# Kernel tuning notes

Measured on AMD Instinct MI355X. Metric: run time of the kernel, lower is better.

The kernel has to match this reference:

```python
import jax, jax.numpy as jnp
import numpy as np

HOP_NUM = 3
N_NODES = 40000
N_EDGES = 640000
IN_DIM = 128
N_ALPHAS = HOP_NUM * (HOP_NUM + 1) // 2  # triangular layerRegular params


def setup_inputs() -> dict:
    key = jax.random.key(0)
    k_h, k_d, k_a, k_s, k_t = jax.random.split(key, 5)
    h = jax.random.normal(k_h, (N_NODES, IN_DIM), dtype=jnp.float32)
    d = jax.random.uniform(k_d, (N_NODES,), dtype=jnp.float32)  # degree normalization per node
    alphas = jax.random.uniform(k_a, (N_ALPHAS,), dtype=jnp.float32)
    src = jax.random.randint(k_s, (N_EDGES,), 0, N_NODES, dtype=jnp.int32)
    dst = jax.random.randint(k_t, (N_EDGES,), 0, N_NODES, dtype=jnp.int32)
    return {"h": h, "d": d, "alphas": alphas, "src": src, "dst": dst}


def reference(h, d, alphas, src, dst):
    n = h.shape[0]
    # edge_applying: e = 1 * d[dst] * d[src]  (symmetric-normalized edge weight)
    e = d[dst] * d[src]                      # [E]
    outs = [h]
    k = 0
    for i in range(HOP_NUM):
        feat = h
        for q in range(i + 1):
            # update_all(u_mul_e('h','e'), sum): agg[v] = sum_{(u,v)} feat[u] * e
            msg = feat[src] * e[:, None]     # [E, D]
            agg = jax.ops.segment_sum(msg, dst, num_segments=n)  # [N, D]
            a = alphas[k]; k += 1
            feat = agg * a + (1.0 - a) * feat
            # feature_drop with p=0.0 (eval) is identity
        outs.append(feat)
    return jnp.concatenate(outs, axis=1)       # [N, (HOP_NUM+1)*D]
```

## Files before the change

kernel.cpp:

```cpp
#include <hip/hip_runtime.h>


#define NN  40000
#define NE  640000
#define CAP 64

__device__ inline unsigned short f2h(float f) {
    _Float16 h = (_Float16)f;
    return *(unsigned short*)&h;
}
__device__ inline float h2f(unsigned short u) {
    _Float16 h = *(_Float16*)&u;
    return (float)h;
}
__device__ inline unsigned short f2bf(float f) {
    unsigned int x = __float_as_uint(f);
    x += 0x7fffu + ((x >> 16) & 1u);
    return (unsigned short)(x >> 16);
}
__device__ inline unsigned int pack_bf2(float x, float y) {
    return ((unsigned int)f2bf(y) << 16) | (unsigned int)f2bf(x);
}
__device__ inline float bflo(unsigned int u) { return __uint_as_float(u << 16); }
__device__ inline float bfhi(unsigned int u) { return __uint_as_float(u & 0xffff0000u); }

__global__ __launch_bounds__(256) void build_buckets_k(
    const int* __restrict__ src, const int* __restrict__ dst,
    const float* __restrict__ deg,
    int* __restrict__ counts, unsigned int* __restrict__ buck) {
    int e = blockIdx.x * 256 + threadIdx.x;
    if (e >= NE) return;
    int s = src[e];
    int v = dst[e];
    int slot = atomicAdd(&counts[v], 1);
    if (slot < CAP) {
        float w = deg[s] * deg[v];
        buck[v * CAP + slot] = ((unsigned int)f2h(w) << 16) | (unsigned int)s;
    }
}

__global__ __launch_bounds__(256) void cvt_h_k(
    const float* __restrict__ h, unsigned int* __restrict__ hb) {
    int i = blockIdx.x * 256 + threadIdx.x;
    if (i >= NN * 64) return;
    float2 f = *(const float2*)(h + (size_t)i * 2);
    hb[i] = pack_bf2(f.x, f.y);
}

__device__ inline float2 gather_node(
    const unsigned int* __restrict__ feat,
    const int* __restrict__ counts, const unsigned int* __restrict__ buck,
    int v, int lane) {
    int cnt = counts[v];
    if (cnt > CAP) cnt = CAP;
    unsigned int myw = buck[(size_t)v * CAP + lane];
    if (lane >= cnt) myw = 0u;
    float ax = 0.f, ay = 0.f, bx = 0.f, by = 0.f;
    for (int j = 0; j < cnt; j += 4) {
        unsigned int u0 = __shfl(myw, j + 0);
        unsigned int u1 = __shfl(myw, j + 1);
        unsigned int u2 = __shfl(myw, j + 2);
        unsigned int u3 = __shfl(myw, j + 3);
        unsigned int f0 = feat[(size_t)(u0 & 0xffffu) * 64 + lane];
        unsigned int f1 = feat[(size_t)(u1 & 0xffffu) * 64 + lane];
        unsigned int f2 = feat[(size_t)(u2 & 0xffffu) * 64 + lane];
        unsigned int f3 = feat[(size_t)(u3 & 0xffffu) * 64 + lane];
        float w0 = h2f((unsigned short)(u0 >> 16));
        float w1 = h2f((unsigned short)(u1 >> 16));
        float w2 = h2f((unsigned short)(u2 >> 16));
        float w3 = h2f((unsigned short)(u3 >> 16));
        ax = fmaf(w0, bflo(f0), ax); ay = fmaf(w0, bfhi(f0), ay);
        bx = fmaf(w1, bflo(f1), bx); by = fmaf(w1, bfhi(f1), by);
        ax = fmaf(w2, bflo(f2), ax); ay = fmaf(w2, bfhi(f2), ay);
        bx = fmaf(w3, bflo(f3), bx); by = fmaf(w3, bfhi(f3), by);
    }
    return make_float2(ax + bx, ay + by);
}

__global__ __launch_bounds__(256) void agg_k(
    const unsigned int* __restrict__ feat,
    const int* __restrict__ counts, const unsigned int* __restrict__ buck,
    unsigned int* __restrict__ outf) {
    int gid  = blockIdx.x * 256 + threadIdx.x;
    int v    = gid >> 6;
    int lane = gid & 63;
    if (v >= NN) return;
    float2 acc = gather_node(feat, counts, buck, v, lane);
    outf[(size_t)v * 64 + lane] = pack_bf2(acc.x, acc.y);
}

__global__ __launch_bounds__(256) void agg3_fused_k(
    const unsigned int* __restrict__ p2b,
    const float* __restrict__ h,
    const unsigned int* __restrict__ p1b,
    const int* __restrict__ counts, const unsigned int* __restrict__ buck,
    const float* __restrict__ alphas, float* __restrict__ out) {
    int gid  = blockIdx.x * 256 + threadIdx.x;
    int v    = gid >> 6;
    int lane = gid & 63;
    if (v >= NN) return;
    float2 p3 = gather_node(p2b, counts, buck, v, lane);

    float a0 = alphas[0], a1 = alphas[1], a2 = alphas[2];
    float a3 = alphas[3], a4 = alphas[4], a5 = alphas[5];
    float c1p = a0, c1h = 1.f - a0;
    float c2pp = a2 * a1;
    float c2p  = a2 * (1.f - a1) + (1.f - a2) * a1;
    float c2h  = (1.f - a2) * (1.f - a1);
    float s2pp = a4 * a3;
    float s2p  = a4 * (1.f - a3) + (1.f - a4) * a3;
    float s2h  = (1.f - a4) * (1.f - a3);
    float c3ppp = a5 * s2pp;
    float c3pp  = a5 * s2p + (1.f - a5) * s2pp;
    float c3p   = a5 * s2h + (1.f - a5) * s2p;
    float c3h   = (1.f - a5) * s2h;

    int i2 = lane * 2;
    float2 hf = *(const float2*)(h + (size_t)v * 128 + i2);
    unsigned int u1 = p1b[(size_t)v * 64 + lane];
    unsigned int u2 = p2b[(size_t)v * 64 + lane];
    float q1x = bflo(u1), q1y = bfhi(u1);
    float q2x = bflo(u2), q2y = bfhi(u2);

    float2 r1, r2, r3;
    r1.x = c1p * q1x + c1h * hf.x;
    r1.y = c1p * q1y + c1h * hf.y;
    r2.x = c2pp * q2x + c2p * q1x + c2h * hf.x;
    r2.y = c2pp * q2y + c2p * q1y + c2h * hf.y;
    r3.x = c3ppp * p3.x + c3pp * q2x + c3p * q1x + c3h * hf.x;
    r3.y = c3ppp * p3.y + c3pp * q2y + c3p * q1y + c3h * hf.y;

    float* o = out + (size_t)v * 512;
    *(float2*)(o + i2)       = hf;
    *(float2*)(o + 128 + i2) = r1;
    *(float2*)(o + 256 + i2) = r2;
    *(float2*)(o + 384 + i2) = r3;
}

extern "C" void kernel_launch(void* const* d_in, const int* in_sizes, int n_in,
                              void* d_out, int out_size, void* d_ws, size_t ws_size,
                              hipStream_t stream) {
    const float* h      = (const float*)d_in[0];
    const float* deg    = (const float*)d_in[1];
    const float* alphas = (const float*)d_in[2];
    const int*   src    = (const int*)d_in[3];
    const int*   dst    = (const int*)d_in[4];
    float* out = (float*)d_out;

    char* ws = (char*)d_ws;
    int*          counts = (int*)(ws + 0);
    unsigned int* buck   = (unsigned int*)(ws + 160000);
    unsigned int* hb     = (unsigned int*)(ws + 10400000);
    unsigned int* p1b    = (unsigned int*)(ws + 20640000);
    unsigned int* p2b    = (unsigned int*)(ws + 30880000);

    hipMemsetAsync(counts, 0, NN * sizeof(int), stream);
    build_buckets_k<<<NE / 256, 256, 0, stream>>>(src, dst, deg, counts, buck);
    cvt_h_k<<<(NN * 64 + 255) / 256, 256, 0, stream>>>(h, hb);

    agg_k<<<NN / 4, 256, 0, stream>>>(hb,  counts, buck, p1b);
    agg_k<<<NN / 4, 256, 0, stream>>>(p1b, counts, buck, p2b);
    agg3_fused_k<<<NN / 4, 256, 0, stream>>>(p2b, h, p1b, counts, buck,
                                             alphas, out);
}
```

Measured before the change: 216.1 us.

## Merge bucket build with bf16 conversion and use scalar bucket loads in gather

Fuses the edge-bucketing kernel and the bf16 conversion of h into a single launch by partitioning the grid by block index, which removes one kernel launch. In the gather, the node index is made wave-uniform with readfirstlane, so bucket entries are read as uniform (scalar) loads instead of a per-lane load followed by shuffles. The loop is unrolled to 8 neighbours with four accumulator pairs to keep more feature loads in flight. Out-of-range slots are masked to node 0 with zero weight, which adds some wasted loads when a bucket count is not a multiple of 8.

Result: no change. 212.4 us (-1.7%).

```diff
diff --git a/kernel.cpp b/kernel.cpp
--- a/kernel.cpp
+++ b/kernel.cpp
@@ -24,57 +24,69 @@
 __device__ inline float bflo(unsigned int u) { return __uint_as_float(u << 16); }
 __device__ inline float bfhi(unsigned int u) { return __uint_as_float(u & 0xffff0000u); }
 
-__global__ __launch_bounds__(256) void build_buckets_k(
+__global__ __launch_bounds__(256) void build_cvt_k(
     const int* __restrict__ src, const int* __restrict__ dst,
-    const float* __restrict__ deg,
-    int* __restrict__ counts, unsigned int* __restrict__ buck) {
-    int e = blockIdx.x * 256 + threadIdx.x;
-    if (e >= NE) return;
-    int s = src[e];
-    int v = dst[e];
-    int slot = atomicAdd(&counts[v], 1);
-    if (slot < CAP) {
-        float w = deg[s] * deg[v];
-        buck[v * CAP + slot] = ((unsigned int)f2h(w) << 16) | (unsigned int)s;
+    const float* __restrict__ deg, const float* __restrict__ h,
+    int* __restrict__ counts, unsigned int* __restrict__ buck,
+    unsigned int* __restrict__ hb) {
+    int b = blockIdx.x;
+    if (b < NE / 256) {
+        int e = b * 256 + threadIdx.x;
+        int s = src[e];
+        int v = dst[e];
+        int slot = atomicAdd(&counts[v], 1);
+        if (slot < CAP) {
+            float w = deg[s] * deg[v];
+            buck[v * CAP + slot] = ((unsigned int)f2h(w) << 16) | (unsigned int)s;
+        }
+    } else {
+        int i = (b - NE / 256) * 256 + threadIdx.x;
+        if (i < NN * 64) {
+            float2 f = *(const float2*)(h + (size_t)i * 2);
+            hb[i] = pack_bf2(f.x, f.y);
+        }
     }
-}
-
-__global__ __launch_bounds__(256) void cvt_h_k(
-    const float* __restrict__ h, unsigned int* __restrict__ hb) {
-    int i = blockIdx.x * 256 + threadIdx.x;
-    if (i >= NN * 64) return;
-    float2 f = *(const float2*)(h + (size_t)i * 2);
-    hb[i] = pack_bf2(f.x, f.y);
 }
 
 __device__ inline float2 gather_node(
     const unsigned int* __restrict__ feat,
     const int* __restrict__ counts, const unsigned int* __restrict__ buck,
     int v, int lane) {
-    int cnt = counts[v];
+    int vs = __builtin_amdgcn_readfirstlane(v);
+    int cnt = counts[vs];
     if (cnt > CAP) cnt = CAP;
-    unsigned int myw = buck[(size_t)v * CAP + lane];
-    if (lane >= cnt) myw = 0u;
+    const unsigned int* brow = buck + (size_t)vs * CAP;
+
     float ax = 0.f, ay = 0.f, bx = 0.f, by = 0.f;
-    for (int j = 0; j < cnt; j += 4) {
-        unsigned int u0 = __shfl(myw, j + 0);
-        unsigned int u1 = __shfl(myw, j + 1);
-        unsigned int u2 = __shfl(myw, j + 2);
-        unsigned int u3 = __shfl(myw, j + 3);
-        unsigned int f0 = feat[(size_t)(u0 & 0xffffu) * 64 + lane];
-        unsigned int f1 = feat[(size_t)(u1 & 0xffffu) * 64 + lane];
-        unsigned int f2 = feat[(size_t)(u2 & 0xffffu) * 64 + lane];
-        unsigned int f3 = feat[(size_t)(u3 & 0xffffu) * 64 + lane];
-        float w0 = h2f((unsigned short)(u0 >> 16));
-        float w1 = h2f((unsigned short)(u1 >> 16));
-        float w2 = h2f((unsigned short)(u2 >> 16));
-        float w3 = h2f((unsigned short)(u3 >> 16));
-        ax = fmaf(w0, bflo(f0), ax); ay = fmaf(w0, bfhi(f0), ay);
-        bx = fmaf(w1, bflo(f1), bx); by = fmaf(w1, bfhi(f1), by);
-        ax = fmaf(w2, bflo(f2), ax); ay = fmaf(w2, bfhi(f2), ay);
-        bx = fmaf(w3, bflo(f3), bx); by = fmaf(w3, bfhi(f3), by);
+    float cx = 0.f, cy = 0.f, dx = 0.f, dy = 0.f;
+    for (int j = 0; j < cnt; j += 8) {
+        unsigned int uu[8];
+#pragma unroll
+        for (int k = 0; k < 8; ++k) uu[k] = brow[j + k];
+        float wj[8]; int sj[8];
+#pragma unroll
+        for (int k = 0; k < 8; ++k) {
+            bool ok = (j + k) < cnt;
+            wj[k] = ok ? h2f((unsigned short)(uu[k] >> 16)) : 0.f;
+            sj[k] = ok ? (int)(uu[k] & 0xffffu) : 0;
+        }
+        unsigned int fj[8];
+#pragma unroll
+        for (int k = 0; k < 8; ++k)
+            fj[k] = feat[(size_t)sj[k] * 64 + lane];
+#pragma unroll
+        for (int k = 0; k < 8; k += 4) {
+            ax = fmaf(wj[k + 0], bflo(fj[k + 0]), ax);
+            ay = fmaf(wj[k + 0], bfhi(fj[k + 0]), ay);
+            bx = fmaf(wj[k + 1], bflo(fj[k + 1]), bx);
+            by = fmaf(wj[k + 1], bfhi(fj[k + 1]), by);
+            cx = fmaf(wj[k + 2], bflo(fj[k + 2]), cx);
+            cy = fmaf(wj[k + 2], bfhi(fj[k + 2]), cy);
+            dx = fmaf(wj[k + 3], bflo(fj[k + 3]), dx);
+            dy = fmaf(wj[k + 3], bfhi(fj[k + 3]), dy);
+        }
     }
-    return make_float2(ax + bx, ay + by);
+    return make_float2((ax + bx) + (cx + dx), (ay + by) + (cy + dy));
 }
 
 __global__ __launch_bounds__(256) void agg_k(
@@ -155,8 +167,8 @@
     unsigned int* p2b    = (unsigned int*)(ws + 30880000);
 
     hipMemsetAsync(counts, 0, NN * sizeof(int), stream);
-    build_buckets_k<<<NE / 256, 256, 0, stream>>>(src, dst, deg, counts, buck);
-    cvt_h_k<<<(NN * 64 + 255) / 256, 256, 0, stream>>>(h, hb);
+    build_cvt_k<<<NE / 256 + (NN * 64 + 255) / 256, 256, 0, stream>>>(
+        src, dst, deg, h, counts, buck, hb);
 
     agg_k<<<NN / 4, 256, 0, stream>>>(hb,  counts, buck, p1b);
     agg_k<<<NN / 4, 256, 0, stream>>>(p1b, counts, buck, p2b);
```

## Split bf16 feature tables into column chunks so gathers stay cache-resident

Applied to the files above, without the earlier changes.

Stores the bf16 node features as four 32-column chunk tables of 8-byte entries and assigns blocks so that the gather for each chunk touches a smaller working set (about 2.5 MB per chunk), aiming for better L2/MALL hit rates. Each node is now handled by 8 lanes per chunk instead of a full wave, with bucket entries read directly in pairs rather than broadcast by shuffles. Nontemporal loads and stores are used for streaming edge lists, buckets and output. The bucket list is re-read once per chunk, and the block-index mapping interleaves chunks, which may spread concurrent work across chunks and weaken the locality it aims for.

Result: slower. 295.4 us (+36.7%).

```diff
diff --git a/kernel.cpp b/kernel.cpp
--- a/kernel.cpp
+++ b/kernel.cpp
@@ -4,6 +4,12 @@
 #define NN  40000
 #define NE  640000
 #define CAP 64
+#define NCH 4
+#define CW  8
+
+typedef unsigned int uint;
+typedef unsigned long long u64;
+typedef float f32x4 __attribute__((ext_vector_type(4)));
 
 __device__ inline unsigned short f2h(float f) {
     _Float16 h = (_Float16)f;
@@ -14,92 +20,98 @@
     return (float)h;
 }
 __device__ inline unsigned short f2bf(float f) {
-    unsigned int x = __float_as_uint(f);
+    uint x = __float_as_uint(f);
     x += 0x7fffu + ((x >> 16) & 1u);
     return (unsigned short)(x >> 16);
 }
-__device__ inline unsigned int pack_bf2(float x, float y) {
-    return ((unsigned int)f2bf(y) << 16) | (unsigned int)f2bf(x);
+__device__ inline uint pack_bf2(float x, float y) {
+    return ((uint)f2bf(y) << 16) | (uint)f2bf(x);
 }
-__device__ inline float bflo(unsigned int u) { return __uint_as_float(u << 16); }
-__device__ inline float bfhi(unsigned int u) { return __uint_as_float(u & 0xffff0000u); }
+__device__ inline float bflo(uint u) { return __uint_as_float(u << 16); }
+__device__ inline float bfhi(uint u) { return __uint_as_float(u & 0xffff0000u); }
 
-__global__ __launch_bounds__(256) void build_buckets_k(
+__global__ __launch_bounds__(256) void build_k(
     const int* __restrict__ src, const int* __restrict__ dst,
     const float* __restrict__ deg,
-    int* __restrict__ counts, unsigned int* __restrict__ buck) {
+    int* __restrict__ counts, uint* __restrict__ buck) {
     int e = blockIdx.x * 256 + threadIdx.x;
-    if (e >= NE) return;
-    int s = src[e];
-    int v = dst[e];
+    int s = __builtin_nontemporal_load(src + e);
+    int v = __builtin_nontemporal_load(dst + e);
     int slot = atomicAdd(&counts[v], 1);
     if (slot < CAP) {
         float w = deg[s] * deg[v];
-        buck[v * CAP + slot] = ((unsigned int)f2h(w) << 16) | (unsigned int)s;
+        __builtin_nontemporal_store(((uint)f2h(w) << 16) | (uint)s,
+                                    &buck[v * CAP + slot]);
     }
 }
 
-__global__ __launch_bounds__(256) void cvt_h_k(
-    const float* __restrict__ h, unsigned int* __restrict__ hb) {
-    int i = blockIdx.x * 256 + threadIdx.x;
-    if (i >= NN * 64) return;
-    float2 f = *(const float2*)(h + (size_t)i * 2);
-    hb[i] = pack_bf2(f.x, f.y);
+__global__ __launch_bounds__(256) void cvt_k(
+    const float* __restrict__ h, u64* __restrict__ tab) {
+    int b  = blockIdx.x;
+    int c  = (b & 7) >> 1;
+    int wi = (b >> 3) * 2 + (b & 1);
+    int t  = wi * 256 + threadIdx.x;
+    int v  = t >> 3, w8 = t & 7;
+    f32x4 hv = __builtin_nontemporal_load(
+        (const f32x4*)(h + (size_t)v * 128 + c * 32 + w8 * 4));
+    u64 o = ((u64)pack_bf2(hv.z, hv.w) << 32) | (u64)pack_bf2(hv.x, hv.y);
+    tab[(size_t)c * NN * CW + t] = o;
 }
 
-__device__ inline float2 gather_node(
-    const unsigned int* __restrict__ feat,
-    const int* __restrict__ counts, const unsigned int* __restrict__ buck,
-    int v, int lane) {
+__device__ inline void gather_chunk(
+    const u64* __restrict__ tab, const int* __restrict__ counts,
+    const uint* __restrict__ buck, int v, int w8, float acc[4]) {
     int cnt = counts[v];
     if (cnt > CAP) cnt = CAP;
-    unsigned int myw = buck[(size_t)v * CAP + lane];
-    if (lane >= cnt) myw = 0u;
-    float ax = 0.f, ay = 0.f, bx = 0.f, by = 0.f;
-    for (int j = 0; j < cnt; j += 4) {
-        unsigned int u0 = __shfl(myw, j + 0);
-        unsigned int u1 = __shfl(myw, j + 1);
-        unsigned int u2 = __shfl(myw, j + 2);
-        unsigned int u3 = __shfl(myw, j + 3);
-        unsigned int f0 = feat[(size_t)(u0 & 0xffffu) * 64 + lane];
-        unsigned int f1 = feat[(size_t)(u1 & 0xffffu) * 64 + lane];
-        unsigned int f2 = feat[(size_t)(u2 & 0xffffu) * 64 + lane];
-        unsigned int f3 = feat[(size_t)(u3 & 0xffffu) * 64 + lane];
-        float w0 = h2f((unsigned short)(u0 >> 16));
-        float w1 = h2f((unsigned short)(u1 >> 16));
-        float w2 = h2f((unsigned short)(u2 >> 16));
-        float w3 = h2f((unsigned short)(u3 >> 16));
-        ax = fmaf(w0, bflo(f0), ax); ay = fmaf(w0, bfhi(f0), ay);
-        bx = fmaf(w1, bflo(f1), bx); by = fmaf(w1, bfhi(f1), by);
-        ax = fmaf(w2, bflo(f2), ax); ay = fmaf(w2, bfhi(f2), ay);
-        bx = fmaf(w3, bflo(f3), bx); by = fmaf(w3, bfhi(f3), by);
+    const u64* brow = (const u64*)(buck + (size_t)v * CAP);
+    acc[0] = acc[1] = acc[2] = acc[3] = 0.f;
+    for (int j = 0; j < cnt; j += 2) {
+        u64 b01 = __builtin_nontemporal_load(brow + (j >> 1));
+        uint b0 = (uint)b01, b1 = (uint)(b01 >> 32);
+        bool ok1 = (j + 1) < cnt;
+        float w0 = h2f((unsigned short)(b0 >> 16));
+        float w1 = ok1 ? h2f((unsigned short)(b1 >> 16)) : 0.f;
+        int s0 = (int)(b0 & 0xffffu);
+        int s1 = ok1 ? (int)(b1 & 0xffffu) : 0;
+        u64 f0 = tab[(size_t)s0 * CW + w8];
+        u64 f1 = tab[(size_t)s1 * CW + w8];
+        uint f0l = (uint)f0, f0h = (uint)(f0 >> 32);
+        uint f1l = (uint)f1, f1h = (uint)(f1 >> 32);
+        acc[0] = fmaf(w0, bflo(f0l), acc[0]); acc[1] = fmaf(w0, bfhi(f0l), acc[1]);
+        acc[2] = fmaf(w0, bflo(f0h), acc[2]); acc[3] = fmaf(w0, bfhi(f0h), acc[3]);
+        acc[0] = fmaf(w1, bflo(f1l), acc[0]); acc[1] = fmaf(w1, bfhi(f1l), acc[1]);
+        acc[2] = fmaf(w1, bflo(f1h), acc[2]); acc[3] = fmaf(w1, bfhi(f1h), acc[3]);
     }
-    return make_float2(ax + bx, ay + by);
 }
 
 __global__ __launch_bounds__(256) void agg_k(
-    const unsigned int* __restrict__ feat,
-    const int* __restrict__ counts, const unsigned int* __restrict__ buck,
-    unsigned int* __restrict__ outf) {
-    int gid  = blockIdx.x * 256 + threadIdx.x;
-    int v    = gid >> 6;
-    int lane = gid & 63;
-    if (v >= NN) return;
-    float2 acc = gather_node(feat, counts, buck, v, lane);
-    outf[(size_t)v * 64 + lane] = pack_bf2(acc.x, acc.y);
+    const u64* __restrict__ tabs_in, const int* __restrict__ counts,
+    const uint* __restrict__ buck, u64* __restrict__ tabs_out) {
+    int b  = blockIdx.x;
+    int c  = (b & 7) >> 1;
+    int wi = (b >> 3) * 2 + (b & 1);
+    int lane = threadIdx.x & 63, wave = threadIdx.x >> 6;
+    int q = lane >> 3, w8 = lane & 7;
+    int v = wi * 32 + wave * 8 + q;
+    float acc[4];
+    gather_chunk(tabs_in + (size_t)c * NN * CW, counts, buck, v, w8, acc);
+    u64 o = ((u64)pack_bf2(acc[2], acc[3]) << 32) | (u64)pack_bf2(acc[0], acc[1]);
+    tabs_out[(size_t)c * NN * CW + (size_t)v * CW + w8] = o;
 }
 
-__global__ __launch_bounds__(256) void agg3_fused_k(
-    const unsigned int* __restrict__ p2b,
-    const float* __restrict__ h,
-    const unsigned int* __restrict__ p1b,
-    const int* __restrict__ counts, const unsigned int* __restrict__ buck,
-    const float* __restrict__ alphas, float* __restrict__ out) {
-    int gid  = blockIdx.x * 256 + threadIdx.x;
-    int v    = gid >> 6;
-    int lane = gid & 63;
-    if (v >= NN) return;
-    float2 p3 = gather_node(p2b, counts, buck, v, lane);
+__global__ __launch_bounds__(256) void agg3_k(
+    const u64* __restrict__ p2t, const u64* __restrict__ p1t,
+    const float* __restrict__ h, const int* __restrict__ counts,
+    const uint* __restrict__ buck, const float* __restrict__ alphas,
+    float* __restrict__ out) {
+    int b  = blockIdx.x;
+    int c  = (b & 7) >> 1;
+    int wi = (b >> 3) * 2 + (b & 1);
+    int lane = threadIdx.x & 63, wave = threadIdx.x >> 6;
+    int q = lane >> 3, w8 = lane & 7;
+    int v = wi * 32 + wave * 8 + q;
+    float p3[4];
+    gather_chunk(p2t + (size_t)c * NN * CW, counts, buck, v, w8, p3);
 
     float a0 = alphas[0], a1 = alphas[1], a2 = alphas[2];
     float a3 = alphas[3], a4 = alphas[4], a5 = alphas[5];
@@ -115,26 +127,29 @@
     float c3p   = a5 * s2h + (1.f - a5) * s2p;
     float c3h   = (1.f - a5) * s2h;
 
-    int i2 = lane * 2;
-    float2 hf = *(const float2*)(h + (size_t)v * 128 + i2);
-    unsigned int u1 = p1b[(size_t)v * 64 + lane];
-    unsigned int u2 = p2b[(size_t)v * 64 + lane];
-    float q1x = bflo(u1), q1y = bfhi(u1);
-    float q2x = bflo(u2), q2y = bfhi(u2);
+    size_t idx = (size_t)c * NN * CW + (size_t)v * CW + w8;
+    u64 u1 = p1t[idx], u2 = p2t[idx];
+    float q1v[4] = { bflo((uint)u1), bfhi((uint)u1),
+                     bflo((uint)(u1 >> 32)), bfhi((uint)(u1 >> 32)) };
+    float q2v[4] = { bflo((uint)u2), bfhi((uint)u2),
+                     bflo((uint)(u2 >> 32)), bfhi((uint)(u2 >> 32)) };
+    f32x4 hv = __builtin_nontemporal_load(
+        (const f32x4*)(h + (size_t)v * 128 + c * 32 + w8 * 4));
+    float hf[4] = { hv.x, hv.y, hv.z, hv.w };
 
-    float2 r1, r2, r3;
-    r1.x = c1p * q1x + c1h * hf.x;
-    r1.y = c1p * q1y + c1h * hf.y;
-    r2.x = c2pp * q2x + c2p * q1x + c2h * hf.x;
-    r2.y = c2pp * q2y + c2p * q1y + c2h * hf.y;
-    r3.x = c3ppp * p3.x + c3pp * q2x + c3p * q1x + c3h * hf.x;
-    r3.y = c3ppp * p3.y + c3pp * q2y + c3p * q1y + c3h * hf.y;
+    f32x4 r1, r2, r3;
+#pragma unroll
+    for (int k = 0; k < 4; ++k) {
+        r1[k] = c1p * q1v[k] + c1h * hf[k];
+        r2[k] = c2pp * q2v[k] + c2p * q1v[k] + c2h * hf[k];
+        r3[k] = c3ppp * p3[k] + c3pp * q2v[k] + c3p * q1v[k] + c3h * hf[k];
+    }
 
-    float* o = out + (size_t)v * 512;
-    *(float2*)(o + i2)       = hf;
-    *(float2*)(o + 128 + i2) = r1;
-    *(float2*)(o + 256 + i2) = r2;
-    *(float2*)(o + 384 + i2) = r3;
+    float* o = out + (size_t)v * 512 + c * 32 + w8 * 4;
+    __builtin_nontemporal_store(hv, (f32x4*)(o));
+    __builtin_nontemporal_store(r1, (f32x4*)(o + 128));
+    __builtin_nontemporal_store(r2, (f32x4*)(o + 256));
+    __builtin_nontemporal_store(r3, (f32x4*)(o + 384));
 }
 
 extern "C" void kernel_launch(void* const* d_in, const int* in_sizes, int n_in,
@@ -148,18 +163,18 @@
     float* out = (float*)d_out;
 
     char* ws = (char*)d_ws;
-    int*          counts = (int*)(ws + 0);
-    unsigned int* buck   = (unsigned int*)(ws + 160000);
-    unsigned int* hb     = (unsigned int*)(ws + 10400000);
-    unsigned int* p1b    = (unsigned int*)(ws + 20640000);
-    unsigned int* p2b    = (unsigned int*)(ws + 30880000);
+    int*  counts = (int*)(ws + 0);
+    uint* buck   = (uint*)(ws + 160000);
+    u64*  hb     = (u64*)(ws + 10400000);
+    u64*  p1b    = (u64*)(ws + 20640000);
+    u64*  p2b    = (u64*)(ws + 30880000);
 
     hipMemsetAsync(counts, 0, NN * sizeof(int), stream);
-    build_buckets_k<<<NE / 256, 256, 0, stream>>>(src, dst, deg, counts, buck);
-    cvt_h_k<<<(NN * 64 + 255) / 256, 256, 0, stream>>>(h, hb);
+    build_k<<<NE / 256, 256, 0, stream>>>(src, dst, deg, counts, buck);
+    cvt_k<<<NN * NCH * CW / 256, 256, 0, stream>>>(h, hb);
 
-    agg_k<<<NN / 4, 256, 0, stream>>>(hb,  counts, buck, p1b);
-    agg_k<<<NN / 4, 256, 0, stream>>>(p1b, counts, buck, p2b);
-    agg3_fused_k<<<NN / 4, 256, 0, stream>>>(p2b, h, p1b, counts, buck,
-                                             alphas, out);
+    agg_k<<<NN * NCH / 32, 256, 0, stream>>>(hb,  counts, buck, p1b);
+    agg_k<<<NN * NCH / 32, 256, 0, stream>>>(p1b, counts, buck, p2b);
+    agg3_k<<<NN * NCH / 32, 256, 0, stream>>>(p2b, p1b, h, counts, buck,
+                                              alphas, out);
 }
```
